# Performance work log

Hardware: AMD Instinct MI355X
Metric: run time of the kernel (lower is better)

The kernel has to match this reference:

```python
import jax, jax.numpy as jnp
import numpy as np

N = 50000        # nodes
K = 16           # neighbors per node
F_IN = 140       # raw feature dim
H, D = 8, 16     # heads, head_dim -> hidden 128
L = 2            # GAT layers
HID = H * D
NEG_SLOPE = 0.2  # LeakyReLU slope in standard GAT


def setup_inputs() -> dict:
    key = jax.random.key(0)
    ks = jax.random.split(key, 8)
    feature = jax.random.normal(ks[0], (N, F_IN), dtype=jnp.float32)
    nb_id = jax.random.randint(ks[1], (N, K), 0, N)
    pca_w = jax.random.normal(ks[2], (F_IN, HID), dtype=jnp.float32) * (1.0 / np.sqrt(F_IN))
    pca_b = jax.random.normal(ks[3], (HID,), dtype=jnp.float32) * 0.01
    Ws = jax.random.normal(ks[4], (L, HID, HID), dtype=jnp.float32) * (1.0 / np.sqrt(HID))
    bs = jax.random.normal(ks[5], (L, HID), dtype=jnp.float32) * 0.01
    a_src = jax.random.normal(ks[6], (L, H, D), dtype=jnp.float32) * (1.0 / np.sqrt(D))
    a_dst = jax.random.normal(ks[7], (L, H, D), dtype=jnp.float32) * (1.0 / np.sqrt(D))
    return {"feature": feature, "nb_id": nb_id, "pca_w": pca_w, "pca_b": pca_b,
            "Ws": Ws, "bs": bs, "a_src": a_src, "a_dst": a_dst}


def _gat_layer(x, nb_id, W, b, asrc, adst):
    # x: [N, HID] -> per-head features h: [N, H, D]
    h = (x @ W + b).reshape(-1, H, D)
    s_src = jnp.einsum('nhd,hd->nh', h, asrc)          # [N, H]
    s_dst = jnp.einsum('nhd,hd->nh', h, adst)          # [N, H]
    # attention logits over K neighbors: [N, K, H]
    e = jax.nn.leaky_relu(s_src[:, None, :] + s_dst[nb_id], NEG_SLOPE)
    alpha = jax.nn.softmax(e, axis=1)                  # softmax over neighbors
    # gather neighbor features [N, K, H, D] and aggregate
    out = jnp.einsum('nkh,nkhd->nhd', alpha, h[nb_id])
    return jax.nn.elu(out.reshape(-1, HID))


def reference(feature, nb_id, pca_w, pca_b, Ws, bs, a_src, a_dst):
    # SparseInput: dropout is identity in eval mode
    x = jax.nn.relu(feature @ pca_w + pca_b)           # [N, HID]
    for l in range(L):
        x = _gat_layer(x, nb_id, Ws[l], bs[l], a_src[l], a_dst[l])
    return x
```

## Files before the change

kernel.cpp:

```cpp
#include <hip/hip_runtime.h>
#include <math.h>

#define NN 50000
#define KK 16
#define FIN 140
#define HH 8
#define HID 128

typedef __attribute__((ext_vector_type(8))) short short8;
typedef __attribute__((ext_vector_type(4))) float f32x4;

__device__ inline unsigned short f2bf(float f) {
  unsigned int u = __float_as_uint(f);
  return (unsigned short)((u + 0x7fffu + ((u >> 16) & 1u)) >> 16);
}
__device__ inline float bf2f(unsigned short h) {
  return __uint_as_float(((unsigned int)h) << 16);
}

__global__ __launch_bounds__(256) void prep_kernel(
    const float* __restrict__ pca_w, const float* __restrict__ Ws,
    unsigned short* __restrict__ frags) {
  const int gid = blockIdx.x * 256 + threadIdx.x;
  const float* W; int K; unsigned short *dh, *dl; int tid;
  if (gid < 20480)      { W = pca_w;          K = FIN; dh = frags;                 dl = dh + 20480; tid = gid; }
  else if (gid < 36864) { W = Ws;             K = HID; dh = frags + 40960;         dl = dh + 16384; tid = gid - 20480; }
  else                  { W = Ws + HID * HID; K = HID; dh = frags + 40960 + 32768; dl = dh + 16384; tid = gid - 36864; }
  const int j = tid & 7, L = (tid >> 3) & 63, ct = tid >> 9, t = ct & 7, c = ct >> 3;
  const int k = c * 32 + (L >> 4) * 8 + j;
  const int col = t * 16 + (L & 15);
  const float v = (k < K) ? W[(size_t)k * HID + col] : 0.f;
  const unsigned short h = f2bf(v);
  dh[tid] = h;
  dl[tid] = f2bf(v - bf2f(h));
}

__device__ inline void split8(const float4& a0, const float4& a1, short8& Ah, short8& Al) {
  const float av[8] = {a0.x, a0.y, a0.z, a0.w, a1.x, a1.y, a1.z, a1.w};
#pragma unroll
  for (int j = 0; j < 8; ++j) {
    const unsigned short hb = f2bf(av[j]);
    Ah[j] = (short)hb;
    Al[j] = (short)f2bf(av[j] - bf2f(hb));
  }
}

__global__ __launch_bounds__(64) void pca_mfma(
    const float* __restrict__ feat, const unsigned short* __restrict__ wfh,
    const unsigned short* __restrict__ wfl, const float* __restrict__ b,
    float* __restrict__ x) {
  const int n0 = blockIdx.x * 16;
  const int lane = threadIdx.x;
  const int col = lane & 15, quad = lane >> 4;
  f32x4 acc[8];
#pragma unroll
  for (int t = 0; t < 8; ++t) acc[t] = (f32x4){0.f, 0.f, 0.f, 0.f};
  const float* arow = feat + (size_t)(n0 + col) * FIN + quad * 8;
#pragma unroll
  for (int c = 0; c < 5; ++c) {
    float4 a0, a1;
    if (c < 4) {
      a0 = *(const float4*)(arow + c * 32);
      a1 = *(const float4*)(arow + c * 32 + 4);
    } else {
      a0 = make_float4(0.f, 0.f, 0.f, 0.f);
      a1 = make_float4(0.f, 0.f, 0.f, 0.f);
      if (quad == 0) { a0 = *(const float4*)(arow + 128); a1 = *(const float4*)(arow + 132); }
      else if (quad == 1) { a0 = *(const float4*)(arow + 128); }
    }
    short8 Ah, Al;
    split8(a0, a1, Ah, Al);
#pragma unroll
    for (int t = 0; t < 8; ++t) {
      const short8 Bh = *(const short8*)(wfh + ((size_t)(c * 8 + t) * 64 + lane) * 8);
      const short8 Bl = *(const short8*)(wfl + ((size_t)(c * 8 + t) * 64 + lane) * 8);
      acc[t] = __builtin_amdgcn_mfma_f32_16x16x32_bf16(Ah, Bl, acc[t], 0, 0, 0);
      acc[t] = __builtin_amdgcn_mfma_f32_16x16x32_bf16(Al, Bh, acc[t], 0, 0, 0);
      acc[t] = __builtin_amdgcn_mfma_f32_16x16x32_bf16(Ah, Bh, acc[t], 0, 0, 0);
    }
  }
#pragma unroll
  for (int t = 0; t < 8; ++t) {
    const float bj = b[t * 16 + col];
#pragma unroll
    for (int r = 0; r < 4; ++r) {
      const float v = acc[t][r] + bj;
      x[(size_t)(n0 + quad * 4 + r) * HID + t * 16 + col] = fmaxf(v, 0.f);
    }
  }
}

__global__ __launch_bounds__(64) void proj_mfma(
    const float* __restrict__ xin, const unsigned short* __restrict__ wfh,
    const unsigned short* __restrict__ wfl, const float* __restrict__ b,
    const float* __restrict__ asrc, const float* __restrict__ adst,
    unsigned short* __restrict__ hbf, float* __restrict__ ssrc,
    float* __restrict__ sdst) {
  const int n0 = blockIdx.x * 16;
  const int lane = threadIdx.x;
  const int col = lane & 15, quad = lane >> 4;
  f32x4 acc[8];
#pragma unroll
  for (int t = 0; t < 8; ++t) acc[t] = (f32x4){0.f, 0.f, 0.f, 0.f};
  const float* arow = xin + (size_t)(n0 + col) * HID + quad * 8;
#pragma unroll
  for (int c = 0; c < 4; ++c) {
    const float4 a0 = *(const float4*)(arow + c * 32);
    const float4 a1 = *(const float4*)(arow + c * 32 + 4);
    short8 Ah, Al;
    split8(a0, a1, Ah, Al);
#pragma unroll
    for (int t = 0; t < 8; ++t) {
      const short8 Bh = *(const short8*)(wfh + ((size_t)(c * 8 + t) * 64 + lane) * 8);
      const short8 Bl = *(const short8*)(wfl + ((size_t)(c * 8 + t) * 64 + lane) * 8);
      acc[t] = __builtin_amdgcn_mfma_f32_16x16x32_bf16(Ah, Bl, acc[t], 0, 0, 0);
      acc[t] = __builtin_amdgcn_mfma_f32_16x16x32_bf16(Al, Bh, acc[t], 0, 0, 0);
      acc[t] = __builtin_amdgcn_mfma_f32_16x16x32_bf16(Ah, Bh, acc[t], 0, 0, 0);
    }
  }
#pragma unroll
  for (int t = 0; t < 8; ++t) {
    const float bj = b[t * 16 + col];
    const float av = asrc[t * 16 + col];
    const float dv = adst[t * 16 + col];
#pragma unroll
    for (int r = 0; r < 4; ++r) {
      const float v = acc[t][r] + bj;
      const int row = n0 + quad * 4 + r;
      hbf[(size_t)row * HID + t * 16 + col] = f2bf(v);
      float vs = v * av;
      float vd = v * dv;
      vs += __shfl_xor(vs, 1, 16); vd += __shfl_xor(vd, 1, 16);
      vs += __shfl_xor(vs, 2, 16); vd += __shfl_xor(vd, 2, 16);
      vs += __shfl_xor(vs, 4, 16); vd += __shfl_xor(vd, 4, 16);
      vs += __shfl_xor(vs, 8, 16); vd += __shfl_xor(vd, 8, 16);
      if (col == 0) {
        ssrc[(size_t)row * HH + t] = vs;
        sdst[(size_t)row * HH + t] = vd;
      }
    }
  }
}

__global__ __launch_bounds__(64) void attn_kernel(
    const int* __restrict__ nb, const unsigned int* __restrict__ hbf,
    const float* __restrict__ ssrc, const float* __restrict__ sdst,
    float* __restrict__ xout) {
  const int n = blockIdx.x;
  const int j = threadIdx.x;
  __shared__ int nbs[KK];
  __shared__ float aw[KK][HH];
  if (j < KK) nbs[j] = nb[(size_t)n * KK + j];
  __syncthreads();
  {
    const int k0 = j >> 3, h0 = j & 7;
    const int k1 = (j + 64) >> 3;
    float e0 = ssrc[(size_t)n * HH + h0] + sdst[(size_t)nbs[k0] * HH + h0];
    float e1 = ssrc[(size_t)n * HH + h0] + sdst[(size_t)nbs[k1] * HH + h0];
    aw[k0][h0] = e0 > 0.f ? e0 : 0.2f * e0;
    aw[k1][h0] = e1 > 0.f ? e1 : 0.2f * e1;
  }
  __syncthreads();
  if (j < HH) {
    float m = -1e30f;
#pragma unroll
    for (int k = 0; k < KK; ++k) m = fmaxf(m, aw[k][j]);
    float s = 0.f;
#pragma unroll
    for (int k = 0; k < KK; ++k) {
      const float v = __expf(aw[k][j] - m);
      aw[k][j] = v;
      s += v;
    }
    const float inv = 1.f / s;
#pragma unroll
    for (int k = 0; k < KK; ++k) aw[k][j] *= inv;
  }
  __syncthreads();
  const int head = j >> 3;
  float acc0 = 0.f, acc1 = 0.f;
#pragma unroll
  for (int k = 0; k < KK; ++k) {
    const unsigned int u = hbf[(size_t)nbs[k] * (HID / 2) + j];
    const float a = aw[k][head];
    acc0 = fmaf(a, __uint_as_float(u << 16), acc0);
    acc1 = fmaf(a, __uint_as_float(u & 0xffff0000u), acc1);
  }
  float2 o;
  o.x = acc0 > 0.f ? acc0 : expm1f(acc0);
  o.y = acc1 > 0.f ? acc1 : expm1f(acc1);
  *(float2*)&xout[(size_t)n * HID + 2 * j] = o;
}

extern "C" void kernel_launch(void* const* d_in, const int* in_sizes, int n_in,
                              void* d_out, int out_size, void* d_ws, size_t ws_size,
                              hipStream_t stream) {
  const float* feature = (const float*)d_in[0];
  const int*   nb      = (const int*)d_in[1];
  const float* pca_w   = (const float*)d_in[2];
  const float* pca_b   = (const float*)d_in[3];
  const float* Ws      = (const float*)d_in[4];
  const float* bs      = (const float*)d_in[5];
  const float* a_src   = (const float*)d_in[6];
  const float* a_dst   = (const float*)d_in[7];
  float* out = (float*)d_out;

  float* xbuf = (float*)d_ws;
  unsigned short* hbf = (unsigned short*)(xbuf + (size_t)NN * HID);
  float* ssrc = (float*)(hbf + (size_t)NN * HID);
  float* sdst = ssrc + (size_t)NN * HH;
  unsigned short* frags = (unsigned short*)(sdst + (size_t)NN * HH);

  prep_kernel<<<208, 256, 0, stream>>>(pca_w, Ws, frags);
  pca_mfma<<<NN / 16, 64, 0, stream>>>(feature, frags, frags + 20480, pca_b, xbuf);
  for (int l = 0; l < 2; ++l) {
    const unsigned short* wh = frags + 40960 + (size_t)l * 32768;
    proj_mfma<<<NN / 16, 64, 0, stream>>>(
        xbuf, wh, wh + 16384, bs + (size_t)l * HID,
        a_src + (size_t)l * HID, a_dst + (size_t)l * HID, hbf, ssrc, sdst);
    attn_kernel<<<NN, 64, 0, stream>>>(nb, (const unsigned int*)hbf, ssrc, sdst,
                                       (l == 1) ? out : xbuf);
  }
}
```

Baseline: 214.9 us.

## Store activations in bf16, drop activation split, use wave-per-node persistent attention

Intermediate activations are now stored as bf16 instead of fp32, and the GEMMs no longer split the activation into hi/lo parts. This cuts each GEMM from three MFMAs per tile to two and halves the activation memory traffic. The operand roles are swapped so the epilogue writes contiguous packed rows. The attention kernel becomes a grid-stride persistent kernel with one wave per node, doing the softmax with shuffles instead of shared memory and barriers, and issuing all neighbor gathers up front. The cost is lower activation precision, which adds rounding error relative to the fp32 reference.

```diff
diff --git a/kernel.cpp b/kernel.cpp
--- a/kernel.cpp
+++ b/kernel.cpp
@@ -35,63 +35,58 @@
   dl[tid] = f2bf(v - bf2f(h));
 }
 
-__device__ inline void split8(const float4& a0, const float4& a1, short8& Ah, short8& Al) {
-  const float av[8] = {a0.x, a0.y, a0.z, a0.w, a1.x, a1.y, a1.z, a1.w};
-#pragma unroll
-  for (int j = 0; j < 8; ++j) {
-    const unsigned short hb = f2bf(av[j]);
-    Ah[j] = (short)hb;
-    Al[j] = (short)f2bf(av[j] - bf2f(hb));
-  }
-}
-
 __global__ __launch_bounds__(64) void pca_mfma(
     const float* __restrict__ feat, const unsigned short* __restrict__ wfh,
     const unsigned short* __restrict__ wfl, const float* __restrict__ b,
-    float* __restrict__ x) {
+    unsigned short* __restrict__ xbf) {
   const int n0 = blockIdx.x * 16;
   const int lane = threadIdx.x;
   const int col = lane & 15, quad = lane >> 4;
   f32x4 acc[8];
 #pragma unroll
   for (int t = 0; t < 8; ++t) acc[t] = (f32x4){0.f, 0.f, 0.f, 0.f};
-  const float* arow = feat + (size_t)(n0 + col) * FIN + quad * 8;
+  const float* brow = feat + (size_t)(n0 + col) * FIN + quad * 8;
 #pragma unroll
   for (int c = 0; c < 5; ++c) {
     float4 a0, a1;
     if (c < 4) {
-      a0 = *(const float4*)(arow + c * 32);
-      a1 = *(const float4*)(arow + c * 32 + 4);
+      a0 = *(const float4*)(brow + c * 32);
+      a1 = *(const float4*)(brow + c * 32 + 4);
     } else {
       a0 = make_float4(0.f, 0.f, 0.f, 0.f);
       a1 = make_float4(0.f, 0.f, 0.f, 0.f);
-      if (quad == 0) { a0 = *(const float4*)(arow + 128); a1 = *(const float4*)(arow + 132); }
-      else if (quad == 1) { a0 = *(const float4*)(arow + 128); }
-    }
-    short8 Ah, Al;
-    split8(a0, a1, Ah, Al);
+      if (quad == 0) { a0 = *(const float4*)(brow + 128); a1 = *(const float4*)(brow + 132); }
+      else if (quad == 1) { a0 = *(const float4*)(brow + 128); }
+    }
+    short8 Bf;
+    Bf[0] = (short)f2bf(a0.x); Bf[1] = (short)f2bf(a0.y);
+    Bf[2] = (short)f2bf(a0.z); Bf[3] = (short)f2bf(a0.w);
+    Bf[4] = (short)f2bf(a1.x); Bf[5] = (short)f2bf(a1.y);
+    Bf[6] = (short)f2bf(a1.z); Bf[7] = (short)f2bf(a1.w);
 #pragma unroll
     for (int t = 0; t < 8; ++t) {
-      const short8 Bh = *(const short8*)(wfh + ((size_t)(c * 8 + t) * 64 + lane) * 8);
-      const short8 Bl = *(const short8*)(wfl + ((size_t)(c * 8 + t) * 64 + lane) * 8);
-      acc[t] = __builtin_amdgcn_mfma_f32_16x16x32_bf16(Ah, Bl, acc[t], 0, 0, 0);
-      acc[t] = __builtin_amdgcn_mfma_f32_16x16x32_bf16(Al, Bh, acc[t], 0, 0, 0);
-      acc[t] = __builtin_amdgcn_mfma_f32_16x16x32_bf16(Ah, Bh, acc[t], 0, 0, 0);
+      const short8 Ah = *(const short8*)(wfh + ((size_t)(c * 8 + t) * 64 + lane) * 8);
+      const short8 Al = *(const short8*)(wfl + ((size_t)(c * 8 + t) * 64 + lane) * 8);
+      acc[t] = __builtin_amdgcn_mfma_f32_16x16x32_bf16(Al, Bf, acc[t], 0, 0, 0);
+      acc[t] = __builtin_amdgcn_mfma_f32_16x16x32_bf16(Ah, Bf, acc[t], 0, 0, 0);
     }
   }
 #pragma unroll
   for (int t = 0; t < 8; ++t) {
-    const float bj = b[t * 16 + col];
-#pragma unroll
-    for (int r = 0; r < 4; ++r) {
-      const float v = acc[t][r] + bj;
-      x[(size_t)(n0 + quad * 4 + r) * HID + t * 16 + col] = fmaxf(v, 0.f);
-    }
+    const float4 bv = *(const float4*)(b + t * 16 + quad * 4);
+    const float v0 = fmaxf(acc[t][0] + bv.x, 0.f);
+    const float v1 = fmaxf(acc[t][1] + bv.y, 0.f);
+    const float v2 = fmaxf(acc[t][2] + bv.z, 0.f);
+    const float v3 = fmaxf(acc[t][3] + bv.w, 0.f);
+    uint2 pk;
+    pk.x = (unsigned)f2bf(v0) | ((unsigned)f2bf(v1) << 16);
+    pk.y = (unsigned)f2bf(v2) | ((unsigned)f2bf(v3) << 16);
+    *(uint2*)&xbf[(size_t)(n0 + col) * HID + t * 16 + quad * 4] = pk;
   }
 }
 
 __global__ __launch_bounds__(64) void proj_mfma(
-    const float* __restrict__ xin, const unsigned short* __restrict__ wfh,
+    const unsigned short* __restrict__ xbf, const unsigned short* __restrict__ wfh,
     const unsigned short* __restrict__ wfl, const float* __restrict__ b,
     const float* __restrict__ asrc, const float* __restrict__ adst,
     unsigned short* __restrict__ hbf, float* __restrict__ ssrc,
@@ -102,94 +97,93 @@
   f32x4 acc[8];
 #pragma unroll
   for (int t = 0; t < 8; ++t) acc[t] = (f32x4){0.f, 0.f, 0.f, 0.f};
-  const float* arow = xin + (size_t)(n0 + col) * HID + quad * 8;
+  const unsigned short* brow = xbf + (size_t)(n0 + col) * HID + quad * 8;
+  short8 Bf[4];
+#pragma unroll
+  for (int c = 0; c < 4; ++c) Bf[c] = *(const short8*)(brow + c * 32);
 #pragma unroll
   for (int c = 0; c < 4; ++c) {
-    const float4 a0 = *(const float4*)(arow + c * 32);
-    const float4 a1 = *(const float4*)(arow + c * 32 + 4);
-    short8 Ah, Al;
-    split8(a0, a1, Ah, Al);
 #pragma unroll
     for (int t = 0; t < 8; ++t) {
-      const short8 Bh = *(const short8*)(wfh + ((size_t)(c * 8 + t) * 64 + lane) * 8);
-      const short8 Bl = *(const short8*)(wfl + ((size_t)(c * 8 + t) * 64 + lane) * 8);
-      acc[t] = __builtin_amdgcn_mfma_f32_16x16x32_bf16(Ah, Bl, acc[t], 0, 0, 0);
-      acc[t] = __builtin_amdgcn_mfma_f32_16x16x32_bf16(Al, Bh, acc[t], 0, 0, 0);
-      acc[t] = __builtin_amdgcn_mfma_f32_16x16x32_bf16(Ah, Bh, acc[t], 0, 0, 0);
+      const short8 Ah = *(const short8*)(wfh + ((size_t)(c * 8 + t) * 64 + lane) * 8);
+      const short8 Al = *(const short8*)(wfl + ((size_t)(c * 8 + t) * 64 + lane) * 8);
+      acc[t] = __builtin_amdgcn_mfma_f32_16x16x32_bf16(Al, Bf[c], acc[t], 0, 0, 0);
+      acc[t] = __builtin_amdgcn_mfma_f32_16x16x32_bf16(Ah, Bf[c], acc[t], 0, 0, 0);
     }
   }
 #pragma unroll
   for (int t = 0; t < 8; ++t) {
-    const float bj = b[t * 16 + col];
-    const float av = asrc[t * 16 + col];
-    const float dv = adst[t * 16 + col];
-#pragma unroll
-    for (int r = 0; r < 4; ++r) {
-      const float v = acc[t][r] + bj;
-      const int row = n0 + quad * 4 + r;
-      hbf[(size_t)row * HID + t * 16 + col] = f2bf(v);
-      float vs = v * av;
-      float vd = v * dv;
-      vs += __shfl_xor(vs, 1, 16); vd += __shfl_xor(vd, 1, 16);
-      vs += __shfl_xor(vs, 2, 16); vd += __shfl_xor(vd, 2, 16);
-      vs += __shfl_xor(vs, 4, 16); vd += __shfl_xor(vd, 4, 16);
-      vs += __shfl_xor(vs, 8, 16); vd += __shfl_xor(vd, 8, 16);
-      if (col == 0) {
-        ssrc[(size_t)row * HH + t] = vs;
-        sdst[(size_t)row * HH + t] = vd;
-      }
-    }
-  }
-}
-
-__global__ __launch_bounds__(64) void attn_kernel(
+    const float4 bv = *(const float4*)(b + t * 16 + quad * 4);
+    const float4 av = *(const float4*)(asrc + t * 16 + quad * 4);
+    const float4 dv = *(const float4*)(adst + t * 16 + quad * 4);
+    const float v0 = acc[t][0] + bv.x;
+    const float v1 = acc[t][1] + bv.y;
+    const float v2 = acc[t][2] + bv.z;
+    const float v3 = acc[t][3] + bv.w;
+    uint2 pk;
+    pk.x = (unsigned)f2bf(v0) | ((unsigned)f2bf(v1) << 16);
+    pk.y = (unsigned)f2bf(v2) | ((unsigned)f2bf(v3) << 16);
+    *(uint2*)&hbf[(size_t)(n0 + col) * HID + t * 16 + quad * 4] = pk;
+    float ps = v0 * av.x + v1 * av.y + v2 * av.z + v3 * av.w;
+    float pd = v0 * dv.x + v1 * dv.y + v2 * dv.z + v3 * dv.w;
+    ps += __shfl_xor(ps, 16); ps += __shfl_xor(ps, 32);
+    pd += __shfl_xor(pd, 16); pd += __shfl_xor(pd, 32);
+    if (quad == 0) ssrc[(size_t)(n0 + col) * HH + t] = ps;
+    if (quad == 1) sdst[(size_t)(n0 + col) * HH + t] = pd;
+  }
+}
+
+template <bool LAST>
+__global__ __launch_bounds__(256) void attn_kernel(
     const int* __restrict__ nb, const unsigned int* __restrict__ hbf,
     const float* __restrict__ ssrc, const float* __restrict__ sdst,
-    float* __restrict__ xout) {
-  const int n = blockIdx.x;
-  const int j = threadIdx.x;
-  __shared__ int nbs[KK];
-  __shared__ float aw[KK][HH];
-  if (j < KK) nbs[j] = nb[(size_t)n * KK + j];
-  __syncthreads();
-  {
-    const int k0 = j >> 3, h0 = j & 7;
-    const int k1 = (j + 64) >> 3;
-    float e0 = ssrc[(size_t)n * HH + h0] + sdst[(size_t)nbs[k0] * HH + h0];
-    float e1 = ssrc[(size_t)n * HH + h0] + sdst[(size_t)nbs[k1] * HH + h0];
-    aw[k0][h0] = e0 > 0.f ? e0 : 0.2f * e0;
-    aw[k1][h0] = e1 > 0.f ? e1 : 0.2f * e1;
-  }
-  __syncthreads();
-  if (j < HH) {
-    float m = -1e30f;
-#pragma unroll
-    for (int k = 0; k < KK; ++k) m = fmaxf(m, aw[k][j]);
-    float s = 0.f;
+    void* __restrict__ xout) {
+  const int lane = threadIdx.x & 63;
+  const int wid = (blockIdx.x << 2) + (threadIdx.x >> 6);
+  const int nw = gridDim.x << 2;
+  for (int n = wid; n < NN; n += nw) {
+    int nbv = 0;
+    if (lane < KK) nbv = nb[(size_t)n * KK + lane];
+    unsigned int u[KK];
 #pragma unroll
     for (int k = 0; k < KK; ++k) {
-      const float v = __expf(aw[k][j] - m);
-      aw[k][j] = v;
-      s += v;
-    }
+      const int r = __shfl(nbv, k);
+      u[k] = hbf[(size_t)r * (HID / 2) + lane];
+    }
+    const int h = lane & 7, k0 = lane >> 3;
+    const int r0 = __shfl(nbv, k0), r1 = __shfl(nbv, k0 + 8);
+    const float ss = ssrc[(size_t)n * HH + h];
+    float e0 = ss + sdst[(size_t)r0 * HH + h];
+    float e1 = ss + sdst[(size_t)r1 * HH + h];
+    e0 = e0 > 0.f ? e0 : 0.2f * e0;
+    e1 = e1 > 0.f ? e1 : 0.2f * e1;
+    float m = fmaxf(e0, e1);
+    m = fmaxf(m, __shfl_xor(m, 8));
+    m = fmaxf(m, __shfl_xor(m, 16));
+    m = fmaxf(m, __shfl_xor(m, 32));
+    float p0 = __expf(e0 - m), p1 = __expf(e1 - m);
+    float s = p0 + p1;
+    s += __shfl_xor(s, 8); s += __shfl_xor(s, 16); s += __shfl_xor(s, 32);
     const float inv = 1.f / s;
-#pragma unroll
-    for (int k = 0; k < KK; ++k) aw[k][j] *= inv;
-  }
-  __syncthreads();
-  const int head = j >> 3;
-  float acc0 = 0.f, acc1 = 0.f;
-#pragma unroll
-  for (int k = 0; k < KK; ++k) {
-    const unsigned int u = hbf[(size_t)nbs[k] * (HID / 2) + j];
-    const float a = aw[k][head];
-    acc0 = fmaf(a, __uint_as_float(u << 16), acc0);
-    acc1 = fmaf(a, __uint_as_float(u & 0xffff0000u), acc1);
-  }
-  float2 o;
-  o.x = acc0 > 0.f ? acc0 : expm1f(acc0);
-  o.y = acc1 > 0.f ? acc1 : expm1f(acc1);
-  *(float2*)&xout[(size_t)n * HID + 2 * j] = o;
+    p0 *= inv; p1 *= inv;
+    const int head = lane >> 3;
+    float acc0 = 0.f, acc1 = 0.f;
+#pragma unroll
+    for (int k = 0; k < KK; ++k) {
+      const float asel = (k < 8) ? p0 : p1;
+      const float a = __shfl(asel, ((k & 7) << 3) + head);
+      acc0 = fmaf(a, __uint_as_float(u[k] << 16), acc0);
+      acc1 = fmaf(a, __uint_as_float(u[k] & 0xffff0000u), acc1);
+    }
+    const float o0 = acc0 > 0.f ? acc0 : expm1f(acc0);
+    const float o1 = acc1 > 0.f ? acc1 : expm1f(acc1);
+    if (LAST) {
+      *(float2*)((float*)xout + (size_t)n * HID + 2 * lane) = make_float2(o0, o1);
+    } else {
+      ((unsigned int*)xout)[(size_t)n * (HID / 2) + lane] =
+          (unsigned)f2bf(o0) | ((unsigned)f2bf(o1) << 16);
+    }
+  }
 }
 
 extern "C" void kernel_launch(void* const* d_in, const int* in_sizes, int n_in,
@@ -205,20 +199,24 @@
   const float* a_dst   = (const float*)d_in[7];
   float* out = (float*)d_out;
 
-  float* xbuf = (float*)d_ws;
-  unsigned short* hbf = (unsigned short*)(xbuf + (size_t)NN * HID);
+  unsigned short* xbf = (unsigned short*)d_ws;
+  unsigned short* hbf = xbf + (size_t)NN * HID;
   float* ssrc = (float*)(hbf + (size_t)NN * HID);
   float* sdst = ssrc + (size_t)NN * HH;
   unsigned short* frags = (unsigned short*)(sdst + (size_t)NN * HH);
 
   prep_kernel<<<208, 256, 0, stream>>>(pca_w, Ws, frags);
-  pca_mfma<<<NN / 16, 64, 0, stream>>>(feature, frags, frags + 20480, pca_b, xbuf);
+  pca_mfma<<<NN / 16, 64, 0, stream>>>(feature, frags, frags + 20480, pca_b, xbf);
   for (int l = 0; l < 2; ++l) {
     const unsigned short* wh = frags + 40960 + (size_t)l * 32768;
     proj_mfma<<<NN / 16, 64, 0, stream>>>(
-        xbuf, wh, wh + 16384, bs + (size_t)l * HID,
+        xbf, wh, wh + 16384, bs + (size_t)l * HID,
         a_src + (size_t)l * HID, a_dst + (size_t)l * HID, hbf, ssrc, sdst);
-    attn_kernel<<<NN, 64, 0, stream>>>(nb, (const unsigned int*)hbf, ssrc, sdst,
-                                       (l == 1) ? out : xbuf);
-  }
-}
+    if (l == 1)
+      attn_kernel<true><<<2048, 256, 0, stream>>>(nb, (const unsigned int*)hbf,
+                                                  ssrc, sdst, (void*)out);
+    else
+      attn_kernel<false><<<2048, 256, 0, stream>>>(nb, (const unsigned int*)hbf,
+                                                   ssrc, sdst, (void*)xbf);
+  }
+}
```

Measured after the change: 217.1 us. No clear change (+1.0%).
